# Optimization experiments

Measured on AMD Instinct MI355X. Metric: run time of the kernel, lower is better.

## Reference

```python
import math
import jax, jax.numpy as jnp
import numpy as np

B, N, D = 8, 2048, 512


def setup_inputs() -> dict:
    key = jax.random.key(0)
    ks = jax.random.split(key, 9)
    s = 1.0 / math.sqrt(D)
    return {
        "x": jax.random.normal(ks[0], (B, N, D), dtype=jnp.float32),
        "adj": jax.random.uniform(ks[1], (B, N, N), dtype=jnp.float32),
        "Wqk": jax.random.normal(ks[2], (D, D), dtype=jnp.float32) * s,
        "bqk": jax.random.normal(ks[3], (D,), dtype=jnp.float32) * s,
        "Wl": jax.random.normal(ks[4], (D, D), dtype=jnp.float32) * s,
        "bl": jax.random.normal(ks[5], (D,), dtype=jnp.float32) * s,
        "Wr": jax.random.normal(ks[6], (D, D), dtype=jnp.float32) * s,
        "Wd": jax.random.normal(ks[7], (D, 1), dtype=jnp.float32),
        "bd": jax.random.normal(ks[8], (D,), dtype=jnp.float32),
    }


def reference(x, adj, Wqk, bqk, Wl, bl, Wr, Wd, bd):
    # degree gating: sigmoid(Linear(rowsum(adj)))
    deg = jnp.sum(adj, axis=-1, keepdims=True)           # [B, N, 1]
    gate = jax.nn.sigmoid(deg * Wd[:, 0] + bd)           # [B, N, D]
    xg = x * gate
    # sigmoid QK features
    QK = jax.nn.sigmoid(xg @ Wqk.T + bqk)                # [B, N, D]
    scores = jnp.einsum("bnd,bmd->bnm", QK, QK) / math.sqrt(D)
    scores = scores * adj                                # adjacency mask
    attn = scores / (jnp.sum(scores, axis=-1, keepdims=True) + 1e-6)
    out = jnp.einsum("bnm,bmd->bnd", attn, xg)           # aggregate values
    out = out @ Wl.T + bl + xg @ Wr.T                    # left + right branch
    return jax.nn.relu(out)
```

## Files before the change

### kernel.cpp

```cpp
#include <hip/hip_runtime.h>
#include <hip/hip_bf16.h>


typedef __bf16 bf16;
typedef __bf16 bf16x8 __attribute__((ext_vector_type(8)));
typedef float  f32x4  __attribute__((ext_vector_type(4)));

#define Bb 8
#define Nn 2048
#define Dd 512
#define SMEM_BYTES 33792

__device__ __forceinline__ bf16 to_bf16(float f) { return (bf16)f; }
__device__ __forceinline__ float sigmoidf_(float x) { return 1.0f / (1.0f + __expf(-x)); }

__device__ __forceinline__ void gld16(const void* g, void* l) {
    __builtin_amdgcn_global_load_lds(
        (__attribute__((address_space(1))) void*)(void*)g,
        (__attribute__((address_space(3))) void*)l,
        16, 0, 0);
}

__device__ __forceinline__ void gemm_bt_core(
    const bf16* __restrict__ A, const bf16* __restrict__ Bt,
    int lda, int ldb, int K,
    char* As, char* Bs, f32x4 acc[4][4])
{
    const int tid  = threadIdx.x;
    const int lane = tid & 63;
    const int wave = tid >> 6;
    const int wm = (wave >> 1) << 6;
    const int wn = (wave & 1) << 6;

    for (int kt = 0; kt < K; kt += 64) {
#pragma unroll
        for (int i = 0; i < 4; ++i) {
            int ff   = i * 256 + tid;
            int row  = ff >> 3;
            int slot = ff & 7;
            int gch  = slot ^ (row & 7);
            gld16(A  + (size_t)row * lda + kt + gch * 8, As + ff * 16);
            gld16(Bt + (size_t)row * ldb + kt + gch * 8, Bs + ff * 16);
        }
        __syncthreads();
#pragma unroll
        for (int ks = 0; ks < 2; ++ks) {
            bf16x8 af[4], bfr[4];
#pragma unroll
            for (int mi = 0; mi < 4; ++mi) {
                int row  = wm + mi * 16 + (lane & 15);
                int slot = ((ks << 2) + (lane >> 4)) ^ (row & 7);
                af[mi] = *(const bf16x8*)(As + row * 128 + slot * 16);
            }
#pragma unroll
            for (int ni = 0; ni < 4; ++ni) {
                int row  = wn + ni * 16 + (lane & 15);
                int slot = ((ks << 2) + (lane >> 4)) ^ (row & 7);
                bfr[ni] = *(const bf16x8*)(Bs + row * 128 + slot * 16);
            }
#pragma unroll
            for (int mi = 0; mi < 4; ++mi)
#pragma unroll
                for (int ni = 0; ni < 4; ++ni)
                    acc[mi][ni] = __builtin_amdgcn_mfma_f32_16x16x32_bf16(
                        af[mi], bfr[ni], acc[mi][ni], 0, 0, 0);
        }
        __syncthreads();
    }
}

#define GEMM_PROLOGUE()                                  \
    __shared__ __align__(16) char smem[SMEM_BYTES];      \
    char* As = smem;                                     \
    char* Bs = smem + 16384;                             \
    f32x4 acc[4][4];                                     \
    _Pragma("unroll") for (int mi = 0; mi < 4; ++mi)     \
    _Pragma("unroll") for (int ni = 0; ni < 4; ++ni)     \
        acc[mi][ni] = (f32x4){0.f, 0.f, 0.f, 0.f};

template <typename F>
__device__ __forceinline__ void epilogue_rt(f32x4 acc[4][4], char* smem, F&& emit)
{
    const int tid  = threadIdx.x;
    const int lane = tid & 63;
    const int wave = tid >> 6;
    const int wm = (wave >> 1) << 6;
    const int wn = (wave & 1) << 6;
    const int cq = lane >> 4;
    const int cl = lane & 15;
    float* t = (float*)smem;
    const int chunk = tid & 15;
    const int rbase = tid >> 4;
#pragma unroll
    for (int ph = 0; ph < 2; ++ph) {
        __syncthreads();
        if ((wm >> 6) == ph) {
#pragma unroll
            for (int mi = 0; mi < 4; ++mi)
#pragma unroll
                for (int ni = 0; ni < 4; ++ni)
#pragma unroll
                    for (int r = 0; r < 4; ++r) {
                        int lr = mi * 16 + cq * 4 + r;
                        int lc = wn + ni * 16 + cl;
                        t[lr * 132 + lc] = acc[mi][ni][r];
                    }
        }
        __syncthreads();
#pragma unroll
        for (int rr = 0; rr < 4; ++rr) {
            int lr = rr * 16 + rbase;
            f32x4 a = *(const f32x4*)&t[lr * 132 + chunk * 8];
            f32x4 b = *(const f32x4*)&t[lr * 132 + chunk * 8 + 4];
            float v[8] = {a[0], a[1], a[2], a[3], b[0], b[1], b[2], b[3]};
            emit(ph * 64 + lr, chunk * 8, v);
        }
    }
}

__global__ __launch_bounds__(256) void k_castw(
    const float* __restrict__ Wqk, const float* __restrict__ Wl,
    const float* __restrict__ Wr,
    bf16* __restrict__ Wqkb, bf16* __restrict__ Wlb, bf16* __restrict__ Wrb)
{
    int i = blockIdx.x * 256 + threadIdx.x;
    Wqkb[i] = to_bf16(Wqk[i]);
    Wlb[i]  = to_bf16(Wl[i]);
    Wrb[i]  = to_bf16(Wr[i]);
}

__global__ __launch_bounds__(256) void k_gate(
    const float* __restrict__ x, const float* __restrict__ adj,
    const float* __restrict__ Wd, const float* __restrict__ bd,
    bf16* __restrict__ xg)
{
    const int rowg = blockIdx.x;
    const float4* arow = (const float4*)(adj + (size_t)rowg * Nn);
    float4 v0 = arow[threadIdx.x];
    float4 v1 = arow[threadIdx.x + 256];
    float s = v0.x + v0.y + v0.z + v0.w + v1.x + v1.y + v1.z + v1.w;
#pragma unroll
    for (int off = 32; off > 0; off >>= 1) s += __shfl_down(s, off, 64);
    __shared__ float red[4];
    if ((threadIdx.x & 63) == 0) red[threadIdx.x >> 6] = s;
    __syncthreads();
    const float deg = red[0] + red[1] + red[2] + red[3];
#pragma unroll
    for (int d = threadIdx.x; d < Dd; d += 256) {
        float g = sigmoidf_(deg * Wd[d] + bd[d]);
        xg[(size_t)rowg * Dd + d] = to_bf16(x[(size_t)rowg * Dd + d] * g);
    }
}

__global__ __launch_bounds__(256) void k_transpose(
    const bf16* __restrict__ xg, bf16* __restrict__ xgT)
{
    const int b = blockIdx.z, nt = blockIdx.y, dt = blockIdx.x;
    __shared__ bf16 tile[64][66];
    const int c = threadIdx.x & 63, r0 = threadIdx.x >> 6;
    const bf16* src = xg + ((size_t)b * Nn + nt * 64) * Dd + dt * 64;
#pragma unroll
    for (int i = 0; i < 16; ++i) {
        int r = i * 4 + r0;
        tile[r][c] = src[(size_t)r * Dd + c];
    }
    __syncthreads();
    bf16* dst = xgT + ((size_t)b * Dd + dt * 64) * Nn + nt * 64;
#pragma unroll
    for (int i = 0; i < 16; ++i) {
        int r = i * 4 + r0;
        dst[(size_t)r * Nn + c] = tile[c][r];
    }
}

__global__ __launch_bounds__(256) void k_qk_gemm(
    const bf16* __restrict__ xg, const bf16* __restrict__ Wqkb,
    const float* __restrict__ bqk, bf16* __restrict__ QK)
{
    const int blockRow = blockIdx.y * 128;
    const int blockCol = blockIdx.x * 128;
    GEMM_PROLOGUE();
    gemm_bt_core(xg + (size_t)blockRow * Dd, Wqkb + (size_t)blockCol * Dd,
                 Dd, Dd, Dd, As, Bs, acc);
    epilogue_rt(acc, smem, [&](int lr, int lc, float* v) {
        int c = blockCol + lc;
        float4 b0 = *(const float4*)(bqk + c);
        float4 b1 = *(const float4*)(bqk + c + 4);
        float bb[8] = {b0.x, b0.y, b0.z, b0.w, b1.x, b1.y, b1.z, b1.w};
        bf16x8 o;
#pragma unroll
        for (int j = 0; j < 8; ++j) o[j] = to_bf16(sigmoidf_(v[j] + bb[j]));
        *(bf16x8*)(QK + (size_t)(blockRow + lr) * Dd + c) = o;
    });
}

__global__ __launch_bounds__(256) void k_s_gemm(
    const bf16* __restrict__ QK, const float* __restrict__ adj,
    bf16* __restrict__ S, float* __restrict__ denom)
{
    const int b = blockIdx.z;
    const int blockRow = blockIdx.y * 128;
    const int blockCol = blockIdx.x * 128;
    const bf16* Qb = QK + (size_t)b * Nn * Dd;
    GEMM_PROLOGUE();
    gemm_bt_core(Qb + (size_t)blockRow * Dd, Qb + (size_t)blockCol * Dd,
                 Dd, Dd, Dd, As, Bs, acc);
    const float scale = 0.044194173824159216f;
    epilogue_rt(acc, smem, [&](int lr, int lc, float* v) {
        int gRow = blockRow + lr;
        size_t base = ((size_t)b * Nn + gRow) * Nn + blockCol + lc;
        float4 a0 = *(const float4*)(adj + base);
        float4 a1 = *(const float4*)(adj + base + 4);
        float aa[8] = {a0.x, a0.y, a0.z, a0.w, a1.x, a1.y, a1.z, a1.w};
        bf16x8 o;
        float ds = 0.f;
#pragma unroll
        for (int j = 0; j < 8; ++j) {
            float s = v[j] * scale * aa[j];
            bf16 sb = to_bf16(s);
            o[j] = sb;
            ds += (float)sb;
        }
        *(bf16x8*)(S + base) = o;
#pragma unroll
        for (int off = 8; off > 0; off >>= 1) ds += __shfl_xor(ds, off, 16);
        if ((threadIdx.x & 15) == 0) atomicAdd(&denom[b * Nn + gRow], ds);
    });
}

__global__ __launch_bounds__(256) void k_h_gemm(
    const bf16* __restrict__ S, const bf16* __restrict__ xgT,
    const float* __restrict__ denom, bf16* __restrict__ h)
{
    const int b = blockIdx.z;
    const int blockRow = blockIdx.y * 128;
    const int blockCol = blockIdx.x * 128;
    GEMM_PROLOGUE();
    gemm_bt_core(S + ((size_t)b * Nn + blockRow) * Nn,
                 xgT + ((size_t)b * Dd + blockCol) * Nn,
                 Nn, Nn, Nn, As, Bs, acc);
    epilogue_rt(acc, smem, [&](int lr, int lc, float* v) {
        int gRow = blockRow + lr;
        float inv = 1.0f / (denom[b * Nn + gRow] + 1e-6f);
        bf16x8 o;
#pragma unroll
        for (int j = 0; j < 8; ++j) o[j] = to_bf16(v[j] * inv);
        *(bf16x8*)(h + ((size_t)b * Nn + gRow) * Dd + blockCol + lc) = o;
    });
}

__global__ __launch_bounds__(256) void k_out_gemm(
    const bf16* __restrict__ h, const bf16* __restrict__ xg,
    const bf16* __restrict__ Wlb, const bf16* __restrict__ Wrb,
    const float* __restrict__ bl, float* __restrict__ out)
{
    const int blockRow = blockIdx.y * 128;
    const int blockCol = blockIdx.x * 128;
    GEMM_PROLOGUE();
    gemm_bt_core(h  + (size_t)blockRow * Dd, Wlb + (size_t)blockCol * Dd,
                 Dd, Dd, Dd, As, Bs, acc);
    gemm_bt_core(xg + (size_t)blockRow * Dd, Wrb + (size_t)blockCol * Dd,
                 Dd, Dd, Dd, As, Bs, acc);
    epilogue_rt(acc, smem, [&](int lr, int lc, float* v) {
        int c = blockCol + lc;
        float4 b0 = *(const float4*)(bl + c);
        float4 b1 = *(const float4*)(bl + c + 4);
        float bb[8] = {b0.x, b0.y, b0.z, b0.w, b1.x, b1.y, b1.z, b1.w};
        float4 o0, o1;
        o0.x = fmaxf(v[0] + bb[0], 0.f); o0.y = fmaxf(v[1] + bb[1], 0.f);
        o0.z = fmaxf(v[2] + bb[2], 0.f); o0.w = fmaxf(v[3] + bb[3], 0.f);
        o1.x = fmaxf(v[4] + bb[4], 0.f); o1.y = fmaxf(v[5] + bb[5], 0.f);
        o1.z = fmaxf(v[6] + bb[6], 0.f); o1.w = fmaxf(v[7] + bb[7], 0.f);
        float* p = out + (size_t)(blockRow + lr) * Dd + c;
        *(float4*)p = o0;
        *(float4*)(p + 4) = o1;
    });
}

extern "C" void kernel_launch(void* const* d_in, const int* in_sizes, int n_in,
                              void* d_out, int out_size, void* d_ws, size_t ws_size,
                              hipStream_t stream) {
    const float* x   = (const float*)d_in[0];
    const float* adj = (const float*)d_in[1];
    const float* Wqk = (const float*)d_in[2];
    const float* bqk = (const float*)d_in[3];
    const float* Wl  = (const float*)d_in[4];
    const float* bl  = (const float*)d_in[5];
    const float* Wr  = (const float*)d_in[6];
    const float* Wd  = (const float*)d_in[7];
    const float* bd  = (const float*)d_in[8];
    float* out = (float*)d_out;

    char* ws = (char*)d_ws;
    bf16* xg   = (bf16*)ws;  ws += (size_t)Bb * Nn * Dd * 2;
    bf16* xgT  = (bf16*)ws;  ws += (size_t)Bb * Dd * Nn * 2;
    bf16* QK   = (bf16*)ws;  ws += (size_t)Bb * Nn * Dd * 2;
    bf16* S    = (bf16*)ws;  ws += (size_t)Bb * Nn * Nn * 2;
    bf16* Wqkb = (bf16*)ws;  ws += (size_t)Dd * Dd * 2;
    bf16* Wlb  = (bf16*)ws;  ws += (size_t)Dd * Dd * 2;
    bf16* Wrb  = (bf16*)ws;  ws += (size_t)Dd * Dd * 2;
    float* denom = (float*)ws; ws += (size_t)Bb * Nn * 4;
    bf16* h = QK;

    hipMemsetAsync(denom, 0, (size_t)Bb * Nn * sizeof(float), stream);
    k_castw<<<dim3(1024), 256, 0, stream>>>(Wqk, Wl, Wr, Wqkb, Wlb, Wrb);
    k_gate<<<dim3(Bb * Nn), 256, 0, stream>>>(x, adj, Wd, bd, xg);
    k_transpose<<<dim3(Dd / 64, Nn / 64, Bb), 256, 0, stream>>>(xg, xgT);
    k_qk_gemm<<<dim3(Dd / 128, (Bb * Nn) / 128), 256, 0, stream>>>(xg, Wqkb, bqk, QK);
    k_s_gemm<<<dim3(Nn / 128, Nn / 128, Bb), 256, 0, stream>>>(QK, adj, S, denom);
    k_h_gemm<<<dim3(Dd / 128, Nn / 128, Bb), 256, 0, stream>>>(S, xgT, denom, h);
    k_out_gemm<<<dim3(Dd / 128, (Bb * Nn) / 128), 256, 0, stream>>>(h, xg, Wlb, Wrb, bl, out);
}
```

Baseline: 404.6 us.

## Exploit QK·QKᵀ symmetry in score GEMM and remap h-GEMM blocks per XCD

```diff
diff --git a/kernel.cpp b/kernel.cpp
--- a/kernel.cpp
+++ b/kernel.cpp
@@ -198,43 +198,99 @@
     const bf16* __restrict__ QK, const float* __restrict__ adj,
     bf16* __restrict__ S, float* __restrict__ denom)
 {
-    const int b = blockIdx.z;
-    const int blockRow = blockIdx.y * 128;
-    const int blockCol = blockIdx.x * 128;
+    const int b = blockIdx.y;
+    int t = blockIdx.x, i = 0;
+    while (t >= 16 - i) { t -= 16 - i; ++i; }
+    const int j = i + t;
+    const int rowI = i * 128, rowJ = j * 128;
     const bf16* Qb = QK + (size_t)b * Nn * Dd;
     GEMM_PROLOGUE();
-    gemm_bt_core(Qb + (size_t)blockRow * Dd, Qb + (size_t)blockCol * Dd,
+    gemm_bt_core(Qb + (size_t)rowI * Dd, Qb + (size_t)rowJ * Dd,
                  Dd, Dd, Dd, As, Bs, acc);
     const float scale = 0.044194173824159216f;
-    epilogue_rt(acc, smem, [&](int lr, int lc, float* v) {
-        int gRow = blockRow + lr;
-        size_t base = ((size_t)b * Nn + gRow) * Nn + blockCol + lc;
-        float4 a0 = *(const float4*)(adj + base);
-        float4 a1 = *(const float4*)(adj + base + 4);
-        float aa[8] = {a0.x, a0.y, a0.z, a0.w, a1.x, a1.y, a1.z, a1.w};
-        bf16x8 o;
-        float ds = 0.f;
-#pragma unroll
-        for (int j = 0; j < 8; ++j) {
-            float s = v[j] * scale * aa[j];
-            bf16 sb = to_bf16(s);
-            o[j] = sb;
-            ds += (float)sb;
-        }
-        *(bf16x8*)(S + base) = o;
-#pragma unroll
-        for (int off = 8; off > 0; off >>= 1) ds += __shfl_xor(ds, off, 16);
-        if ((threadIdx.x & 15) == 0) atomicAdd(&denom[b * Nn + gRow], ds);
-    });
+
+    const int tid  = threadIdx.x;
+    const int lane = tid & 63;
+    const int wave = tid >> 6;
+    const int wm = (wave >> 1) << 6;
+    const int wn = (wave & 1) << 6;
+    const int cq = lane >> 4;
+    const int cl = lane & 15;
+    float* tls = (float*)smem;
+    const int chunk = tid & 15;
+    const int rbase = tid >> 4;
+
+    auto store_side = [&](int blockRow, int blockCol, bool trans) {
+#pragma unroll
+        for (int ph = 0; ph < 2; ++ph) {
+            __syncthreads();
+            if (!trans) {
+                if ((wave >> 1) == ph) {
+#pragma unroll
+                    for (int mi = 0; mi < 4; ++mi)
+#pragma unroll
+                        for (int ni = 0; ni < 4; ++ni)
+#pragma unroll
+                            for (int r = 0; r < 4; ++r)
+                                tls[(mi * 16 + cq * 4 + r) * 132 + wn + ni * 16 + cl]
+                                    = acc[mi][ni][r];
+                }
+            } else {
+                if ((wave & 1) == ph) {
+#pragma unroll
+                    for (int mi = 0; mi < 4; ++mi)
+#pragma unroll
+                        for (int ni = 0; ni < 4; ++ni)
+#pragma unroll
+                            for (int r = 0; r < 4; ++r)
+                                tls[(ni * 16 + cl) * 132 + wm + mi * 16 + cq * 4 + r]
+                                    = acc[mi][ni][r];
+                }
+            }
+            __syncthreads();
+#pragma unroll
+            for (int rr = 0; rr < 4; ++rr) {
+                int lr = rr * 16 + rbase;
+                f32x4 a = *(const f32x4*)&tls[lr * 132 + chunk * 8];
+                f32x4 c4 = *(const f32x4*)&tls[lr * 132 + chunk * 8 + 4];
+                float v[8] = {a[0], a[1], a[2], a[3], c4[0], c4[1], c4[2], c4[3]};
+                int gRow = blockRow + ph * 64 + lr;
+                size_t base = ((size_t)b * Nn + gRow) * Nn + blockCol + chunk * 8;
+                float4 a0 = *(const float4*)(adj + base);
+                float4 a1 = *(const float4*)(adj + base + 4);
+                float aa[8] = {a0.x, a0.y, a0.z, a0.w, a1.x, a1.y, a1.z, a1.w};
+                bf16x8 o;
+                float ds = 0.f;
+#pragma unroll
+                for (int jj = 0; jj < 8; ++jj) {
+                    float s = v[jj] * scale * aa[jj];
+                    bf16 sb = to_bf16(s);
+                    o[jj] = sb;
+                    ds += (float)sb;
+                }
+                *(bf16x8*)(S + base) = o;
+#pragma unroll
+                for (int off = 8; off > 0; off >>= 1) ds += __shfl_xor(ds, off, 16);
+                if ((tid & 15) == 0) atomicAdd(&denom[b * Nn + gRow], ds);
+            }
+        }
+    };
+    store_side(rowI, rowJ, false);
+    if (i != j) store_side(rowJ, rowI, true);
 }
 
 __global__ __launch_bounds__(256) void k_h_gemm(
     const bf16* __restrict__ S, const bf16* __restrict__ xgT,
     const float* __restrict__ denom, bf16* __restrict__ h)
 {
-    const int b = blockIdx.z;
-    const int blockRow = blockIdx.y * 128;
-    const int blockCol = blockIdx.x * 128;
+    const int id  = blockIdx.x;
+    const int xcd = id & 7;
+    const int pos = id >> 3;
+    const int xt  = pos & 3;
+    const int rg  = xcd * 16 + (pos >> 2);
+    const int b   = rg >> 4;
+    const int blockRow = (rg & 15) * 128;
+    const int blockCol = xt * 128;
     GEMM_PROLOGUE();
     gemm_bt_core(S + ((size_t)b * Nn + blockRow) * Nn,
                  xgT + ((size_t)b * Dd + blockCol) * Nn,
@@ -307,7 +363,7 @@
     k_gate<<<dim3(Bb * Nn), 256, 0, stream>>>(x, adj, Wd, bd, xg);
     k_transpose<<<dim3(Dd / 64, Nn / 64, Bb), 256, 0, stream>>>(xg, xgT);
     k_qk_gemm<<<dim3(Dd / 128, (Bb * Nn) / 128), 256, 0, stream>>>(xg, Wqkb, bqk, QK);
-    k_s_gemm<<<dim3(Nn / 128, Nn / 128, Bb), 256, 0, stream>>>(QK, adj, S, denom);
-    k_h_gemm<<<dim3(Dd / 128, Nn / 128, Bb), 256, 0, stream>>>(S, xgT, denom, h);
+    k_s_gemm<<<dim3(136, Bb), 256, 0, stream>>>(QK, adj, S, denom);
+    k_h_gemm<<<dim3(512), 256, 0, stream>>>(S, xgT, denom, h);
     k_out_gemm<<<dim3(Dd / 128, (Bb * Nn) / 128), 256, 0, stream>>>(h, xg, Wlb, Wrb, bl, out);
 }
```

Result: faster. 388.9 us (-3.9%).
